# Performance work log

Measured on AMD Instinct MI355X. Metric: run time of the kernel, lower is better.

The kernel has to match this reference:

```python
import jax, jax.numpy as jnp
import numpy as np

TEMPERATURE = 0.07
EPS = 1e-8
B, D, C = 4096, 512, 10


def setup_inputs() -> dict:
    key = jax.random.key(0)
    k1, k2 = jax.random.split(key)
    features = jax.random.normal(k1, (B, D), dtype=jnp.float32)
    cls = jax.random.randint(k2, (B,), 0, C)
    labels = jax.nn.one_hot(cls, C, dtype=jnp.float32)  # [B, C] one-hot
    return {"features": features, "labels": labels}


def reference(features, labels):
    b = features.shape[0]
    # L2-normalize rows
    feats = features / jnp.linalg.norm(features, axis=1, keepdims=True)
    sim = jnp.clip(feats @ feats.T / TEMPERATURE, -20.0, 20.0)  # [B, B]
    eye = jnp.eye(b, dtype=bool)
    sim = jnp.where(eye, -jnp.inf, sim)  # mask self-similarity

    labels_norm = labels / (labels.sum(axis=1, keepdims=True) + EPS)
    label_sim = labels_norm @ labels_norm.T  # [B, B]
    label_sim = jnp.where(eye, 0.0, label_sim)
    pos_mask = label_sim > 0.1  # [B, B] bool

    exp_sim = jnp.exp(sim)  # diag -> exp(-inf) = 0
    pos_sum = jnp.sum(jnp.where(pos_mask, exp_sim, 0.0), axis=1)  # [B]
    all_sum = jnp.sum(exp_sim, axis=1)  # diag already zero => off-diagonal sum
    loss_i = -jnp.log(pos_sum / (all_sum + EPS) + EPS)  # [B]

    valid = jnp.any(pos_mask, axis=1)  # rows with >=1 positive
    n_valid = jnp.sum(valid.astype(jnp.float32))
    total = jnp.sum(jnp.where(valid, loss_i, 0.0))
    return jnp.where(n_valid > 0, total / n_valid, 0.0)
```

## Files before the change

kernel.cpp:

```cpp
#include <hip/hip_runtime.h>
#include <stdint.h>


#define B_ROWS 4096
#define D_DIM  512
#define C_CLS  10
#define NT     32

typedef __bf16 bf16x8 __attribute__((ext_vector_type(8)));
typedef float  f32x4  __attribute__((ext_vector_type(4)));

__device__ __forceinline__ void load_lds16(const __bf16* g, __bf16* l) {
  __builtin_amdgcn_global_load_lds(
      (const __attribute__((address_space(1))) unsigned int*)g,
      (__attribute__((address_space(3))) unsigned int*)l,
      16, 0, 0);
}

__global__ __launch_bounds__(256) void prep_kernel(
    const float* __restrict__ feats, const float* __restrict__ labels,
    __bf16* __restrict__ F, int* __restrict__ cls,
    float* __restrict__ pos_sum, float* __restrict__ all_sum) {
  const int w = threadIdx.x >> 6, lane = threadIdx.x & 63;
  const int row = blockIdx.x * 4 + w;
  const float* fr = feats + (size_t)row * D_DIM;
  float4 v0 = ((const float4*)fr)[2 * lane];
  float4 v1 = ((const float4*)fr)[2 * lane + 1];
  float ss = v0.x*v0.x + v0.y*v0.y + v0.z*v0.z + v0.w*v0.w
           + v1.x*v1.x + v1.y*v1.y + v1.z*v1.z + v1.w*v1.w;
  #pragma unroll
  for (int m = 1; m < 64; m <<= 1) ss += __shfl_xor(ss, m, 64);
  float inv = 1.0f / sqrtf(ss);

  bf16x8 o;
  o[0] = (__bf16)(v0.x * inv); o[1] = (__bf16)(v0.y * inv);
  o[2] = (__bf16)(v0.z * inv); o[3] = (__bf16)(v0.w * inv);
  o[4] = (__bf16)(v1.x * inv); o[5] = (__bf16)(v1.y * inv);
  o[6] = (__bf16)(v1.z * inv); o[7] = (__bf16)(v1.w * inv);
  *(bf16x8*)(F + (size_t)row * D_DIM + 8 * lane) = o;

  float lv = (lane < C_CLS) ? labels[(size_t)row * C_CLS + lane] : 0.f;
  unsigned long long m = __ballot(lv > 0.5f);
  if (lane == 0) {
    cls[row] = (int)(__ffsll((long long)m) - 1);
    pos_sum[row] = 0.f;
    all_sum[row] = 0.f;
  }
}

__global__ __launch_bounds__(256) void sim_kernel(
    const __bf16* __restrict__ F, const int* __restrict__ cls,
    float* __restrict__ pos_sum, float* __restrict__ all_sum) {
  __shared__ __align__(16) __bf16 Abuf[128 * 64];
  __shared__ __align__(16) __bf16 Bbuf[128 * 64];
  __shared__ int clsA[128], clsB[128];

  int rem = blockIdx.x, bi = 0, rowlen = NT;
  while (rem >= rowlen) { rem -= rowlen; ++bi; --rowlen; }
  const int bj = bi + rem;
  const int i0 = bi * 128, j0 = bj * 128;
  const bool offdiag = (bi != bj);

  const int tid = threadIdx.x;
  const int w = tid >> 6, lane = tid & 63;
  const int wi = w & 1, wj = w >> 1;
  const int q = lane >> 4, cl = lane & 15;

  if (tid < 128) clsA[tid] = cls[i0 + tid];
  else           clsB[tid - 128] = cls[j0 + tid - 128];

  f32x4 acc[4][4];
  #pragma unroll
  for (int ri = 0; ri < 4; ++ri)
    #pragma unroll
    for (int cj = 0; cj < 4; ++cj) acc[ri][cj] = (f32x4){0.f, 0.f, 0.f, 0.f};

  const int srow = lane >> 3;
  const int sg   = (lane & 7) ^ srow;

  for (int k0 = 0; k0 < D_DIM; k0 += 64) {
    __syncthreads();
    #pragma unroll
    for (int r = 0; r < 4; ++r) {
      const int rowbase = w * 32 + r * 8;
      const __bf16* ga = F + (size_t)(i0 + rowbase + srow) * D_DIM + k0 + sg * 8;
      const __bf16* gb = F + (size_t)(j0 + rowbase + srow) * D_DIM + k0 + sg * 8;
      load_lds16(ga, &Abuf[rowbase * 64]);
      load_lds16(gb, &Bbuf[rowbase * 64]);
    }
    __syncthreads();

    #pragma unroll
    for (int kk = 0; kk < 64; kk += 32) {
      const int cgbase = (kk >> 3) + q;
      const int cc = cgbase ^ (cl & 7);
      bf16x8 af[4], bf[4];
      #pragma unroll
      for (int ri = 0; ri < 4; ++ri)
        af[ri] = *(const bf16x8*)&Abuf[(64 * wi + 16 * ri + cl) * 64 + cc * 8];
      #pragma unroll
      for (int cj = 0; cj < 4; ++cj)
        bf[cj] = *(const bf16x8*)&Bbuf[(64 * wj + 16 * cj + cl) * 64 + cc * 8];
      #pragma unroll
      for (int ri = 0; ri < 4; ++ri)
        #pragma unroll
        for (int cj = 0; cj < 4; ++cj)
          acc[ri][cj] = __builtin_amdgcn_mfma_f32_16x16x32_bf16(
              af[ri], bf[cj], acc[ri][cj], 0, 0, 0);
    }
  }

  const float invT = 1.0f / 0.07f;
  float cs_all[4] = {0.f, 0.f, 0.f, 0.f};
  float cs_pos[4] = {0.f, 0.f, 0.f, 0.f};

  #pragma unroll
  for (int ri = 0; ri < 4; ++ri) {
    float ra[4] = {0.f, 0.f, 0.f, 0.f};
    float rp[4] = {0.f, 0.f, 0.f, 0.f};
    #pragma unroll
    for (int cj = 0; cj < 4; ++cj) {
      const int jloc = 64 * wj + 16 * cj + cl;
      const int gj = j0 + jloc;
      const int cjc = clsB[jloc];
      #pragma unroll
      for (int r = 0; r < 4; ++r) {
        const int iloc = 64 * wi + 16 * ri + q * 4 + r;
        const int gi = i0 + iloc;
        float s = acc[ri][cj][r] * invT;
        s = fminf(fmaxf(s, -20.f), 20.f);
        const bool diag = (gi == gj);
        float e = diag ? 0.f : __expf(s);
        const bool pos = (!diag) && (cjc == clsA[iloc]);
        ra[r] += e;
        cs_all[cj] += e;
        if (pos) { rp[r] += e; cs_pos[cj] += e; }
      }
    }
    #pragma unroll
    for (int r = 0; r < 4; ++r) {
      float sa = ra[r], sp = rp[r];
      #pragma unroll
      for (int m = 1; m < 16; m <<= 1) {
        sa += __shfl_xor(sa, m, 64);
        sp += __shfl_xor(sp, m, 64);
      }
      if (cl == 0) {
        const int gi = i0 + 64 * wi + 16 * ri + q * 4 + r;
        atomicAdd(&all_sum[gi], sa);
        atomicAdd(&pos_sum[gi], sp);
      }
    }
  }
  if (offdiag) {
    #pragma unroll
    for (int cj = 0; cj < 4; ++cj) {
      float sa = cs_all[cj], sp = cs_pos[cj];
      sa += __shfl_xor(sa, 16, 64); sa += __shfl_xor(sa, 32, 64);
      sp += __shfl_xor(sp, 16, 64); sp += __shfl_xor(sp, 32, 64);
      if (q == 0) {
        const int gj = j0 + 64 * wj + 16 * cj + cl;
        atomicAdd(&all_sum[gj], sa);
        atomicAdd(&pos_sum[gj], sp);
      }
    }
  }
}

__global__ __launch_bounds__(256) void finalize_kernel(
    const float* __restrict__ pos_sum, const float* __restrict__ all_sum,
    float* __restrict__ out) {
  __shared__ float redT[4], redC[4];
  const int t = threadIdx.x;
  float total = 0.f, cnt = 0.f;
  for (int i = t; i < B_ROWS; i += 256) {
    float ps = pos_sum[i], as = all_sum[i];
    if (ps > 0.f) {
      total += -logf(ps / (as + 1e-8f) + 1e-8f);
      cnt += 1.f;
    }
  }
  #pragma unroll
  for (int m = 1; m < 64; m <<= 1) {
    total += __shfl_xor(total, m, 64);
    cnt   += __shfl_xor(cnt, m, 64);
  }
  if ((t & 63) == 0) { redT[t >> 6] = total; redC[t >> 6] = cnt; }
  __syncthreads();
  if (t == 0) {
    float T = 0.f, Cn = 0.f;
    #pragma unroll
    for (int i = 0; i < 4; ++i) { T += redT[i]; Cn += redC[i]; }
    out[0] = (Cn > 0.f) ? (T / Cn) : 0.f;
  }
}

extern "C" void kernel_launch(void* const* d_in, const int* in_sizes, int n_in,
                              void* d_out, int out_size, void* d_ws, size_t ws_size,
                              hipStream_t stream) {
  const float* features = (const float*)d_in[0];
  const float* labels   = (const float*)d_in[1];
  float* out = (float*)d_out;

  __bf16* F      = (__bf16*)d_ws;
  int*    cls    = (int*)((char*)d_ws + (size_t)B_ROWS * D_DIM * 2);
  float*  pos_sum = (float*)((char*)cls + B_ROWS * sizeof(int));
  float*  all_sum = pos_sum + B_ROWS;

  prep_kernel<<<B_ROWS / 4, 256, 0, stream>>>(features, labels, F, cls,
                                              pos_sum, all_sum);
  sim_kernel<<<NT * (NT + 1) / 2, 256, 0, stream>>>(F, cls, pos_sum, all_sum);
  finalize_kernel<<<1, 256, 0, stream>>>(pos_sum, all_sum, out);
}
```

Baseline: 101.8 us.

## Double-buffer LDS tiles and fuse finalize into sim kernel via ticket

The K-loop now uses two LDS buffers, so the global-to-LDS loads for the next 64-wide slice are issued while the MFMAs run on the current slice, with one barrier per iteration instead of two. The separate finalize kernel is removed. The last sim block to finish, found with an atomic ticket counter that prep_kernel resets, computes the loss reduction, which saves one kernel launch. LDS use doubles to 64KB per block, which may lower occupancy.

```diff
diff --git a/kernel.cpp b/kernel.cpp
--- a/kernel.cpp
+++ b/kernel.cpp
@@ -6,6 +6,7 @@
 #define D_DIM  512
 #define C_CLS  10
 #define NT     32
+#define NTILES (NT * (NT + 1) / 2)
 
 typedef __bf16 bf16x8 __attribute__((ext_vector_type(8)));
 typedef float  f32x4  __attribute__((ext_vector_type(4)));
@@ -13,14 +14,14 @@
 __device__ __forceinline__ void load_lds16(const __bf16* g, __bf16* l) {
   __builtin_amdgcn_global_load_lds(
       (const __attribute__((address_space(1))) unsigned int*)g,
-      (__attribute__((address_space(3))) unsigned int*)l,
-      16, 0, 0);
+      (__attribute__((address_space(3))) unsigned int*)l, 16, 0, 0);
 }
 
 __global__ __launch_bounds__(256) void prep_kernel(
     const float* __restrict__ feats, const float* __restrict__ labels,
     __bf16* __restrict__ F, int* __restrict__ cls,
-    float* __restrict__ pos_sum, float* __restrict__ all_sum) {
+    float* __restrict__ pos_sum, float* __restrict__ all_sum,
+    int* __restrict__ done) {
   const int w = threadIdx.x >> 6, lane = threadIdx.x & 63;
   const int row = blockIdx.x * 4 + w;
   const float* fr = feats + (size_t)row * D_DIM;
@@ -46,14 +47,18 @@
     pos_sum[row] = 0.f;
     all_sum[row] = 0.f;
   }
+  if (blockIdx.x == 0 && threadIdx.x == 0) *done = 0;
 }
 
 __global__ __launch_bounds__(256) void sim_kernel(
     const __bf16* __restrict__ F, const int* __restrict__ cls,
-    float* __restrict__ pos_sum, float* __restrict__ all_sum) {
-  __shared__ __align__(16) __bf16 Abuf[128 * 64];
-  __shared__ __align__(16) __bf16 Bbuf[128 * 64];
+    float* __restrict__ pos_sum, float* __restrict__ all_sum,
+    int* __restrict__ done, float* __restrict__ out) {
+  __shared__ __align__(16) __bf16 Abuf[2][128 * 64];
+  __shared__ __align__(16) __bf16 Bbuf[2][128 * 64];
   __shared__ int clsA[128], clsB[128];
+  __shared__ int ticket_s;
+  __shared__ float redv[8];
 
   int rem = blockIdx.x, bi = 0, rowlen = NT;
   while (rem >= rowlen) { rem -= rowlen; ++bi; --rowlen; }
@@ -78,29 +83,34 @@
   const int srow = lane >> 3;
   const int sg   = (lane & 7) ^ srow;
 
-  for (int k0 = 0; k0 < D_DIM; k0 += 64) {
+  #define STAGE(k0, b)                                                        \
+    _Pragma("unroll")                                                         \
+    for (int r = 0; r < 4; ++r) {                                             \
+      const int rowbase = w * 32 + r * 8;                                     \
+      const __bf16* ga = F + (size_t)(i0 + rowbase + srow) * D_DIM + (k0) + sg * 8; \
+      const __bf16* gb = F + (size_t)(j0 + rowbase + srow) * D_DIM + (k0) + sg * 8; \
+      load_lds16(ga, &Abuf[b][rowbase * 64]);                                 \
+      load_lds16(gb, &Bbuf[b][rowbase * 64]);                                 \
+    }
+
+  STAGE(0, 0)
+
+  #pragma unroll
+  for (int k = 0; k < D_DIM / 64; ++k) {
     __syncthreads();
-    #pragma unroll
-    for (int r = 0; r < 4; ++r) {
-      const int rowbase = w * 32 + r * 8;
-      const __bf16* ga = F + (size_t)(i0 + rowbase + srow) * D_DIM + k0 + sg * 8;
-      const __bf16* gb = F + (size_t)(j0 + rowbase + srow) * D_DIM + k0 + sg * 8;
-      load_lds16(ga, &Abuf[rowbase * 64]);
-      load_lds16(gb, &Bbuf[rowbase * 64]);
-    }
-    __syncthreads();
-
+    if (k < D_DIM / 64 - 1) { STAGE((k + 1) * 64, (k + 1) & 1) }
+    const __bf16* Ab = &Abuf[k & 1][0];
+    const __bf16* Bb = &Bbuf[k & 1][0];
     #pragma unroll
     for (int kk = 0; kk < 64; kk += 32) {
-      const int cgbase = (kk >> 3) + q;
-      const int cc = cgbase ^ (cl & 7);
+      const int cc = ((kk >> 3) + q) ^ (cl & 7);
       bf16x8 af[4], bf[4];
       #pragma unroll
       for (int ri = 0; ri < 4; ++ri)
-        af[ri] = *(const bf16x8*)&Abuf[(64 * wi + 16 * ri + cl) * 64 + cc * 8];
+        af[ri] = *(const bf16x8*)&Ab[(64 * wi + 16 * ri + cl) * 64 + cc * 8];
       #pragma unroll
       for (int cj = 0; cj < 4; ++cj)
-        bf[cj] = *(const bf16x8*)&Bbuf[(64 * wj + 16 * cj + cl) * 64 + cc * 8];
+        bf[cj] = *(const bf16x8*)&Bb[(64 * wj + 16 * cj + cl) * 64 + cc * 8];
       #pragma unroll
       for (int ri = 0; ri < 4; ++ri)
         #pragma unroll
@@ -109,6 +119,7 @@
               af[ri], bf[cj], acc[ri][cj], 0, 0, 0);
     }
   }
+  #undef STAGE
 
   const float invT = 1.0f / 0.07f;
   float cs_all[4] = {0.f, 0.f, 0.f, 0.f};
@@ -131,10 +142,9 @@
         s = fminf(fmaxf(s, -20.f), 20.f);
         const bool diag = (gi == gj);
         float e = diag ? 0.f : __expf(s);
-        const bool pos = (!diag) && (cjc == clsA[iloc]);
         ra[r] += e;
         cs_all[cj] += e;
-        if (pos) { rp[r] += e; cs_pos[cj] += e; }
+        if (!diag && cjc == clsA[iloc]) { rp[r] += e; cs_pos[cj] += e; }
       }
     }
     #pragma unroll
@@ -165,33 +175,34 @@
       }
     }
   }
-}
-
-__global__ __launch_bounds__(256) void finalize_kernel(
-    const float* __restrict__ pos_sum, const float* __restrict__ all_sum,
-    float* __restrict__ out) {
-  __shared__ float redT[4], redC[4];
-  const int t = threadIdx.x;
-  float total = 0.f, cnt = 0.f;
-  for (int i = t; i < B_ROWS; i += 256) {
-    float ps = pos_sum[i], as = all_sum[i];
-    if (ps > 0.f) {
-      total += -logf(ps / (as + 1e-8f) + 1e-8f);
-      cnt += 1.f;
-    }
-  }
-  #pragma unroll
-  for (int m = 1; m < 64; m <<= 1) {
-    total += __shfl_xor(total, m, 64);
-    cnt   += __shfl_xor(cnt, m, 64);
-  }
-  if ((t & 63) == 0) { redT[t >> 6] = total; redC[t >> 6] = cnt; }
+
+  __threadfence();
   __syncthreads();
-  if (t == 0) {
-    float T = 0.f, Cn = 0.f;
-    #pragma unroll
-    for (int i = 0; i < 4; ++i) { T += redT[i]; Cn += redC[i]; }
-    out[0] = (Cn > 0.f) ? (T / Cn) : 0.f;
+  if (tid == 0) ticket_s = atomicAdd(done, 1);
+  __syncthreads();
+  if (ticket_s == NTILES - 1) {
+    __threadfence();
+    float total = 0.f, cnt = 0.f;
+    for (int i = tid; i < B_ROWS; i += 256) {
+      float ps = pos_sum[i], as = all_sum[i];
+      if (ps > 0.f) {
+        total += -__logf(ps / (as + 1e-8f) + 1e-8f);
+        cnt += 1.f;
+      }
+    }
+    #pragma unroll
+    for (int m = 1; m < 64; m <<= 1) {
+      total += __shfl_xor(total, m, 64);
+      cnt   += __shfl_xor(cnt, m, 64);
+    }
+    if ((tid & 63) == 0) { redv[tid >> 6] = total; redv[4 + (tid >> 6)] = cnt; }
+    __syncthreads();
+    if (tid == 0) {
+      float T = 0.f, Cn = 0.f;
+      #pragma unroll
+      for (int i = 0; i < 4; ++i) { T += redv[i]; Cn += redv[4 + i]; }
+      out[0] = (Cn > 0.f) ? (T / Cn) : 0.f;
+    }
   }
 }
 
@@ -202,13 +213,13 @@
   const float* labels   = (const float*)d_in[1];
   float* out = (float*)d_out;
 
-  __bf16* F      = (__bf16*)d_ws;
-  int*    cls    = (int*)((char*)d_ws + (size_t)B_ROWS * D_DIM * 2);
+  __bf16* F       = (__bf16*)d_ws;
+  int*    cls     = (int*)((char*)d_ws + (size_t)B_ROWS * D_DIM * 2);
   float*  pos_sum = (float*)((char*)cls + B_ROWS * sizeof(int));
   float*  all_sum = pos_sum + B_ROWS;
+  int*    done    = (int*)(all_sum + B_ROWS);
 
   prep_kernel<<<B_ROWS / 4, 256, 0, stream>>>(features, labels, F, cls,
-                                              pos_sum, all_sum);
-  sim_kernel<<<NT * (NT + 1) / 2, 256, 0, stream>>>(F, cls, pos_sum, all_sum);
-  finalize_kernel<<<1, 256, 0, stream>>>(pos_sum, all_sum, out);
-}
+                                              pos_sum, all_sum, done);
+  sim_kernel<<<NTILES, 256, 0, stream>>>(F, cls, pos_sum, all_sum, done, out);
+}
```

New measurement: 127.7 us. 25.4% more time.

## Replace global atomic row sums with per-tile partials and parallel finalize

Applied to the files above, without the earlier changes.

Each similarity tile now gathers its row and column exp-sums in shared memory and writes them to a per-(tile-row, tile-col) partial buffer instead of issuing global atomics. The finalize step becomes 32 blocks that each reduce the 32 partials for their 128 rows, compute the losses, and atomically add to two totals, followed by a tiny divide kernel. The intent is to remove global atomic contention and the serial single-block finalize. In exchange it adds partial-buffer traffic, an extra kernel launch and shared-memory atomics.

```diff
diff --git a/kernel.cpp b/kernel.cpp
--- a/kernel.cpp
+++ b/kernel.cpp
@@ -1,11 +1,11 @@
 #include <hip/hip_runtime.h>
-#include <stdint.h>
 
 
 #define B_ROWS 4096
 #define D_DIM  512
 #define C_CLS  10
-#define NT     32
+#define NTB    32
+#define NTILES (NTB * (NTB + 1) / 2)
 
 typedef __bf16 bf16x8 __attribute__((ext_vector_type(8)));
 typedef float  f32x4  __attribute__((ext_vector_type(4)));
@@ -13,14 +13,13 @@
 __device__ __forceinline__ void load_lds16(const __bf16* g, __bf16* l) {
   __builtin_amdgcn_global_load_lds(
       (const __attribute__((address_space(1))) unsigned int*)g,
-      (__attribute__((address_space(3))) unsigned int*)l,
-      16, 0, 0);
+      (__attribute__((address_space(3))) unsigned int*)l, 16, 0, 0);
 }
 
 __global__ __launch_bounds__(256) void prep_kernel(
     const float* __restrict__ feats, const float* __restrict__ labels,
     __bf16* __restrict__ F, int* __restrict__ cls,
-    float* __restrict__ pos_sum, float* __restrict__ all_sum) {
+    float* __restrict__ totals) {
   const int w = threadIdx.x >> 6, lane = threadIdx.x & 63;
   const int row = blockIdx.x * 4 + w;
   const float* fr = feats + (size_t)row * D_DIM;
@@ -41,33 +40,32 @@
 
   float lv = (lane < C_CLS) ? labels[(size_t)row * C_CLS + lane] : 0.f;
   unsigned long long m = __ballot(lv > 0.5f);
-  if (lane == 0) {
-    cls[row] = (int)(__ffsll((long long)m) - 1);
-    pos_sum[row] = 0.f;
-    all_sum[row] = 0.f;
-  }
+  if (lane == 0) cls[row] = (int)(__ffsll((long long)m) - 1);
+  if (blockIdx.x == 0 && threadIdx.x == 0) { totals[0] = 0.f; totals[1] = 0.f; }
 }
 
 __global__ __launch_bounds__(256) void sim_kernel(
     const __bf16* __restrict__ F, const int* __restrict__ cls,
-    float* __restrict__ pos_sum, float* __restrict__ all_sum) {
+    float* __restrict__ P_all, float* __restrict__ P_pos) {
   __shared__ __align__(16) __bf16 Abuf[128 * 64];
   __shared__ __align__(16) __bf16 Bbuf[128 * 64];
   __shared__ int clsA[128], clsB[128];
-
-  int rem = blockIdx.x, bi = 0, rowlen = NT;
+  __shared__ float g_row_all[128], g_row_pos[128];
+  __shared__ float g_col_all[128], g_col_pos[128];
+
+  int rem = blockIdx.x, bi = 0, rowlen = NTB;
   while (rem >= rowlen) { rem -= rowlen; ++bi; --rowlen; }
   const int bj = bi + rem;
   const int i0 = bi * 128, j0 = bj * 128;
   const bool offdiag = (bi != bj);
 
-  const int tid = threadIdx.x;
-  const int w = tid >> 6, lane = tid & 63;
+  const int t = threadIdx.x;
+  const int w = t >> 6, lane = t & 63;
   const int wi = w & 1, wj = w >> 1;
   const int q = lane >> 4, cl = lane & 15;
 
-  if (tid < 128) clsA[tid] = cls[i0 + tid];
-  else           clsB[tid - 128] = cls[j0 + tid - 128];
+  if (t < 128) { clsA[t] = cls[i0 + t]; g_row_all[t] = 0.f; g_row_pos[t] = 0.f; }
+  else { clsB[t-128] = cls[j0 + t - 128]; g_col_all[t-128] = 0.f; g_col_pos[t-128] = 0.f; }
 
   f32x4 acc[4][4];
   #pragma unroll
@@ -83,30 +81,29 @@
     #pragma unroll
     for (int r = 0; r < 4; ++r) {
       const int rowbase = w * 32 + r * 8;
-      const __bf16* ga = F + (size_t)(i0 + rowbase + srow) * D_DIM + k0 + sg * 8;
-      const __bf16* gb = F + (size_t)(j0 + rowbase + srow) * D_DIM + k0 + sg * 8;
-      load_lds16(ga, &Abuf[rowbase * 64]);
-      load_lds16(gb, &Bbuf[rowbase * 64]);
+      load_lds16(F + (size_t)(i0 + rowbase + srow) * D_DIM + k0 + sg * 8,
+                 &Abuf[rowbase * 64]);
+      load_lds16(F + (size_t)(j0 + rowbase + srow) * D_DIM + k0 + sg * 8,
+                 &Bbuf[rowbase * 64]);
     }
     __syncthreads();
 
     #pragma unroll
     for (int kk = 0; kk < 64; kk += 32) {
-      const int cgbase = (kk >> 3) + q;
-      const int cc = cgbase ^ (cl & 7);
-      bf16x8 af[4], bf[4];
+      const int cc = ((kk >> 3) + q) ^ (cl & 7);
+      bf16x8 af[4], bfr[4];
       #pragma unroll
       for (int ri = 0; ri < 4; ++ri)
         af[ri] = *(const bf16x8*)&Abuf[(64 * wi + 16 * ri + cl) * 64 + cc * 8];
       #pragma unroll
       for (int cj = 0; cj < 4; ++cj)
-        bf[cj] = *(const bf16x8*)&Bbuf[(64 * wj + 16 * cj + cl) * 64 + cc * 8];
+        bfr[cj] = *(const bf16x8*)&Bbuf[(64 * wj + 16 * cj + cl) * 64 + cc * 8];
       #pragma unroll
       for (int ri = 0; ri < 4; ++ri)
         #pragma unroll
         for (int cj = 0; cj < 4; ++cj)
           acc[ri][cj] = __builtin_amdgcn_mfma_f32_16x16x32_bf16(
-              af[ri], bf[cj], acc[ri][cj], 0, 0, 0);
+              af[ri], bfr[cj], acc[ri][cj], 0, 0, 0);
     }
   }
 
@@ -131,10 +128,9 @@
         s = fminf(fmaxf(s, -20.f), 20.f);
         const bool diag = (gi == gj);
         float e = diag ? 0.f : __expf(s);
-        const bool pos = (!diag) && (cjc == clsA[iloc]);
         ra[r] += e;
         cs_all[cj] += e;
-        if (pos) { rp[r] += e; cs_pos[cj] += e; }
+        if (!diag && cjc == clsA[iloc]) { rp[r] += e; cs_pos[cj] += e; }
       }
     }
     #pragma unroll
@@ -146,9 +142,9 @@
         sp += __shfl_xor(sp, m, 64);
       }
       if (cl == 0) {
-        const int gi = i0 + 64 * wi + 16 * ri + q * 4 + r;
-        atomicAdd(&all_sum[gi], sa);
-        atomicAdd(&pos_sum[gi], sp);
+        const int rloc = 64 * wi + 16 * ri + q * 4 + r;
+        atomicAdd(&g_row_all[rloc], sa);
+        atomicAdd(&g_row_pos[rloc], sp);
       }
     }
   }
@@ -159,40 +155,66 @@
       sa += __shfl_xor(sa, 16, 64); sa += __shfl_xor(sa, 32, 64);
       sp += __shfl_xor(sp, 16, 64); sp += __shfl_xor(sp, 32, 64);
       if (q == 0) {
-        const int gj = j0 + 64 * wj + 16 * cj + cl;
-        atomicAdd(&all_sum[gj], sa);
-        atomicAdd(&pos_sum[gj], sp);
-      }
-    }
+        const int jloc = 64 * wj + 16 * cj + cl;
+        atomicAdd(&g_col_all[jloc], sa);
+        atomicAdd(&g_col_pos[jloc], sp);
+      }
+    }
+  }
+  __syncthreads();
+
+  if (t < 128) {
+    const size_t base_row = ((size_t)bi * NTB + bj) * 128;
+    P_all[base_row + t] = g_row_all[t];
+    P_pos[base_row + t] = g_row_pos[t];
+  } else if (offdiag) {
+    const size_t base_col = ((size_t)bj * NTB + bi) * 128;
+    P_all[base_col + t - 128] = g_col_all[t - 128];
+    P_pos[base_col + t - 128] = g_col_pos[t - 128];
   }
 }
 
 __global__ __launch_bounds__(256) void finalize_kernel(
-    const float* __restrict__ pos_sum, const float* __restrict__ all_sum,
-    float* __restrict__ out) {
-  __shared__ float redT[4], redC[4];
+    const float* __restrict__ P_all, const float* __restrict__ P_pos,
+    float* __restrict__ totals) {
+  __shared__ float Sall[4096], Spos[4096];
+  __shared__ float redL[2], redC[2];
+  const int s = blockIdx.x;
   const int t = threadIdx.x;
-  float total = 0.f, cnt = 0.f;
-  for (int i = t; i < B_ROWS; i += 256) {
-    float ps = pos_sum[i], as = all_sum[i];
-    if (ps > 0.f) {
-      total += -logf(ps / (as + 1e-8f) + 1e-8f);
-      cnt += 1.f;
-    }
-  }
-  #pragma unroll
-  for (int m = 1; m < 64; m <<= 1) {
-    total += __shfl_xor(total, m, 64);
-    cnt   += __shfl_xor(cnt, m, 64);
-  }
-  if ((t & 63) == 0) { redT[t >> 6] = total; redC[t >> 6] = cnt; }
+  for (int i = t; i < 4096; i += 256) {
+    Sall[i] = P_all[(size_t)s * 4096 + i];
+    Spos[i] = P_pos[(size_t)s * 4096 + i];
+  }
+  __syncthreads();
+  if (t < 128) {
+    float a = 0.f, p = 0.f;
+    #pragma unroll 8
+    for (int k = 0; k < 32; ++k) {
+      a += Sall[k * 128 + t];
+      p += Spos[k * 128 + t];
+    }
+    float loss = 0.f, cnt = 0.f;
+    if (p > 0.f) {
+      loss = -logf(p / (a + 1e-8f) + 1e-8f);
+      cnt = 1.f;
+    }
+    #pragma unroll
+    for (int m = 1; m < 64; m <<= 1) {
+      loss += __shfl_xor(loss, m, 64);
+      cnt  += __shfl_xor(cnt, m, 64);
+    }
+    if ((t & 63) == 0) { redL[t >> 6] = loss; redC[t >> 6] = cnt; }
+  }
   __syncthreads();
   if (t == 0) {
-    float T = 0.f, Cn = 0.f;
-    #pragma unroll
-    for (int i = 0; i < 4; ++i) { T += redT[i]; Cn += redC[i]; }
-    out[0] = (Cn > 0.f) ? (T / Cn) : 0.f;
-  }
+    atomicAdd(&totals[0], redL[0] + redL[1]);
+    atomicAdd(&totals[1], redC[0] + redC[1]);
+  }
+}
+
+__global__ void div_kernel(const float* __restrict__ totals,
+                           float* __restrict__ out) {
+  out[0] = (totals[1] > 0.f) ? (totals[0] / totals[1]) : 0.f;
 }
 
 extern "C" void kernel_launch(void* const* d_in, const int* in_sizes, int n_in,
@@ -204,11 +226,12 @@
 
   __bf16* F      = (__bf16*)d_ws;
   int*    cls    = (int*)((char*)d_ws + (size_t)B_ROWS * D_DIM * 2);
-  float*  pos_sum = (float*)((char*)cls + B_ROWS * sizeof(int));
-  float*  all_sum = pos_sum + B_ROWS;
-
-  prep_kernel<<<B_ROWS / 4, 256, 0, stream>>>(features, labels, F, cls,
-                                              pos_sum, all_sum);
-  sim_kernel<<<NT * (NT + 1) / 2, 256, 0, stream>>>(F, cls, pos_sum, all_sum);
-  finalize_kernel<<<1, 256, 0, stream>>>(pos_sum, all_sum, out);
-}
+  float*  P_all  = (float*)((char*)cls + B_ROWS * sizeof(int));
+  float*  P_pos  = P_all + (size_t)NTB * NTB * 128;
+  float*  totals = P_pos + (size_t)NTB * NTB * 128;
+
+  prep_kernel<<<B_ROWS / 4, 256, 0, stream>>>(features, labels, F, cls, totals);
+  sim_kernel<<<NTILES, 256, 0, stream>>>(F, cls, P_all, P_pos);
+  finalize_kernel<<<NTB, 256, 0, stream>>>(P_all, P_pos, totals);
+  div_kernel<<<1, 1, 0, stream>>>(totals, out);
+}
```

Measured after the change: 96.56 us. -5.2%, faster.
